# Kernel tuning notes

Measured on AMD Instinct MI355X. Metric: run time of the kernel, lower is better.

Reference implementation:

```python
import jax, jax.numpy as jnp
import numpy as np

B, S, D_MODEL = 2, 2048, 4096
N_HEADS, N_KV, HEAD_DIM = 32, 8, 128
N_GROUPS = N_HEADS // N_KV
QKV_DIM = (N_HEADS + 2 * N_KV) * HEAD_DIM


def _rope_tables(seq_len, head_dim, base=10000.0):
    inv_freq = 1.0 / (base ** (np.arange(0, head_dim, 2, dtype=np.float32) / head_dim))
    t = np.arange(seq_len, dtype=np.float32)
    freqs = np.outer(t, inv_freq)                      # [S, D/2]
    emb = np.concatenate([freqs, freqs], axis=-1)      # [S, D]
    return jnp.asarray(np.cos(emb)), jnp.asarray(np.sin(emb))


def setup_inputs() -> dict:
    key = jax.random.key(0)
    k1, k2, k3 = jax.random.split(key, 3)
    cos, sin = _rope_tables(S, HEAD_DIM)
    return {
        "hidden_states": jax.random.normal(k1, (B, S, D_MODEL), dtype=jnp.float32),
        "cos": cos,
        "sin": sin,
        "W_qkv": jax.random.normal(k2, (D_MODEL, QKV_DIM), dtype=jnp.float32) * (D_MODEL ** -0.5),
        "W_out": jax.random.normal(k3, (D_MODEL, D_MODEL), dtype=jnp.float32) * (D_MODEL ** -0.5),
    }


def _rotate_half(x):
    x1, x2 = jnp.split(x, 2, axis=-1)
    return jnp.concatenate([-x2, x1], axis=-1)


def _apply_rope(x, cos, sin):
    # x: [b, h, s, d]; cos/sin: [s, d]
    c = cos[None, None, :, :]
    s = sin[None, None, :, :]
    return x * c + _rotate_half(x) * s


def reference(hidden_states, cos, sin, W_qkv, W_out):
    b, s, _ = hidden_states.shape
    qkv = jnp.einsum("bsm,mq->bsq", hidden_states, W_qkv)
    q_end = N_HEADS * HEAD_DIM
    kv_sz = N_KV * HEAD_DIM
    q = qkv[..., :q_end].reshape(b, s, N_HEADS, HEAD_DIM).transpose(0, 2, 1, 3)
    k = qkv[..., q_end:q_end + kv_sz].reshape(b, s, N_KV, HEAD_DIM).transpose(0, 2, 1, 3)
    v = qkv[..., q_end + kv_sz:].reshape(b, s, N_KV, HEAD_DIM).transpose(0, 2, 1, 3)

    q = _apply_rope(q, cos, sin)          # [b, H, s, d]
    k = _apply_rope(k, cos, sin)          # [b, KV, s, d] (equiv. to repeat->rope->stride slice)

    # GQA without materializing repeated KV: group query heads per KV head.
    qg = q.reshape(b, N_KV, N_GROUPS, s, HEAD_DIM)
    scale = HEAD_DIM ** -0.5
    scores = jnp.einsum("bkgqd,bkpd->bkgqp", qg, k) * scale  # [b, KV, G, s, s]
    causal = jnp.tril(jnp.ones((s, s), dtype=bool))
    scores = jnp.where(causal, scores, jnp.finfo(scores.dtype).min)
    probs = jax.nn.softmax(scores, axis=-1)
    out = jnp.einsum("bkgqp,bkpd->bkgqd", probs, v)           # [b, KV, G, s, d]
    out = out.reshape(b, N_HEADS, s, HEAD_DIM).transpose(0, 2, 1, 3).reshape(b, s, D_MODEL)
    return jnp.einsum("bsm,mn->bsn", out, W_out)
```

## Files before the change

kernel.cpp:

```cpp
#include <hip/hip_runtime.h>


typedef __bf16 bf16;
typedef bf16 bf16x8 __attribute__((ext_vector_type(8)));
typedef bf16 bf16x4 __attribute__((ext_vector_type(4)));
typedef float f32x4 __attribute__((ext_vector_type(4)));
typedef unsigned int u32;
typedef u32 u32x4 __attribute__((ext_vector_type(4)));

#define B_ 2
#define S_ 2048
#define DM 4096
#define NH 32
#define NKV 8
#define HD 128
#define QKV_DIM 6144

typedef __attribute__((address_space(3))) void lds_void;
typedef const __attribute__((address_space(1))) void glb_void;

__device__ __forceinline__ void gld_lds16(const bf16* g, bf16* l) {
  __builtin_amdgcn_global_load_lds((glb_void*)g, (lds_void*)l, 16, 0, 0);
}

__device__ __forceinline__ u32 bf16bits(float x) {
  union { bf16 h; unsigned short s; } u;
  u.h = (bf16)x;
  return (u32)u.s;
}

#define BAR() __builtin_amdgcn_s_barrier()
#define VM4() asm volatile("s_waitcnt vmcnt(4)" ::: "memory")
#define VM0() asm volatile("s_waitcnt vmcnt(0)" ::: "memory")
#define PRIO1() __builtin_amdgcn_s_setprio(1)
#define PRIO0() __builtin_amdgcn_s_setprio(0)

__global__ __launch_bounds__(256) void cast_f32_bf16(const float* __restrict__ src,
                                                     bf16* __restrict__ dst, int n) {
  int i = (blockIdx.x * 256 + threadIdx.x) * 4;
  float4 v = *(const float4*)(src + i);
  bf16x4 o;
  o[0] = (bf16)v.x; o[1] = (bf16)v.y; o[2] = (bf16)v.z; o[3] = (bf16)v.w;
  *(bf16x4*)(dst + i) = o;
}

__global__ __launch_bounds__(256) void transpose_cast_w(const float* __restrict__ W,
                                                        bf16* __restrict__ Wt,
                                                        int K, int N) {
  __shared__ float tile[64][65];
  const int n0 = blockIdx.x * 64, k0 = blockIdx.y * 64;
  const int t = threadIdx.x, j = t & 63, i0 = t >> 6;
  for (int p = 0; p < 16; ++p) {
    int i = i0 + p * 4;
    tile[i][j] = W[(size_t)(k0 + i) * N + n0 + j];
  }
  __syncthreads();
  for (int p = 0; p < 16; ++p) {
    int n = i0 + p * 4;
    Wt[(size_t)(n0 + n) * K + k0 + j] = (bf16)tile[j][n];
  }
}

__global__ __launch_bounds__(256) void transpose_v(const bf16* __restrict__ qkv,
                                                   bf16* __restrict__ v_t) {
  __shared__ bf16 tile[64][65];
  const int s0 = blockIdx.x * 64;
  const int d0 = blockIdx.y * 64;
  const int bk = blockIdx.z;
  const int b = bk >> 3, kv = bk & 7;
  const int t = threadIdx.x, j = t & 63, i0 = t >> 6;
  const bf16* src = qkv + (size_t)b * S_ * QKV_DIM + 5120 + kv * HD;
  for (int p = 0; p < 16; ++p) {
    int i = i0 + p * 4;
    tile[i][j] = src[(size_t)(s0 + i) * QKV_DIM + d0 + j];
  }
  __syncthreads();
  bf16* dst = v_t + ((size_t)bk * HD + d0) * S_ + s0;
  for (int p = 0; p < 16; ++p) {
    int dd = i0 + p * 4;
    dst[(size_t)dd * S_ + j] = tile[j][dd];
  }
}

__global__ __launch_bounds__(320) void rope_kernel(const bf16* __restrict__ qkv,
                                                   const float* __restrict__ cosT,
                                                   const float* __restrict__ sinT,
                                                   bf16* __restrict__ q_r,
                                                   bf16* __restrict__ k_r) {
  const int bs = blockIdx.x;
  const int b = bs >> 11, s = bs & 2047;
  const int t = threadIdx.x;
  const int hh = t >> 3;
  const int g = (t & 7) * 8;
  const bool isQ = hh < NH;
  const bf16* row = qkv + (size_t)bs * QKV_DIM + (isQ ? hh * HD : DM + (hh - NH) * HD);
  bf16x8 xl8 = *(const bf16x8*)(row + g);
  bf16x8 xh8 = *(const bf16x8*)(row + g + 64);
  const float* cbase = cosT + (size_t)s * HD;
  const float* sbase = sinT + (size_t)s * HD;
  float cl[8], sl[8], ch[8], sh[8];
  *(float4*)(cl) = *(const float4*)(cbase + g);
  *(float4*)(cl + 4) = *(const float4*)(cbase + g + 4);
  *(float4*)(ch) = *(const float4*)(cbase + g + 64);
  *(float4*)(ch + 4) = *(const float4*)(cbase + g + 68);
  *(float4*)(sl) = *(const float4*)(sbase + g);
  *(float4*)(sl + 4) = *(const float4*)(sbase + g + 4);
  *(float4*)(sh) = *(const float4*)(sbase + g + 64);
  *(float4*)(sh + 4) = *(const float4*)(sbase + g + 68);
  const float scale = isQ ? 0.08838834764831845f : 1.0f;
  bf16x8 ol8, oh8;
#pragma unroll
  for (int j = 0; j < 8; ++j) {
    const float xl = (float)xl8[j], xh = (float)xh8[j];
    ol8[j] = (bf16)((xl * cl[j] - xh * sl[j]) * scale);
    oh8[j] = (bf16)((xh * ch[j] + xl * sh[j]) * scale);
  }
  bf16* dst = isQ ? (q_r + (((size_t)(b * NH + hh)) * S_ + s) * HD)
                  : (k_r + (((size_t)(b * NKV + (hh - NH))) * S_ + s) * HD);
  *(bf16x8*)(dst + g) = ol8;
  *(bf16x8*)(dst + g + 64) = oh8;
}

template <bool OUT_BF16, int BM, int BN>
__global__ __launch_bounds__(512, 2) void gemm_bt(const bf16* __restrict__ A,
                                                  const bf16* __restrict__ Bt,
                                                  void* __restrict__ Cout,
                                                  int M, int N, int K) {
  constexpr int MF = BM / 32;
  constexpr int NF = BN / 64;
  constexpr int NCA = BM / 128;
  constexpr int NCB = BN / 128;
  constexpr int AKH = BM * 64;
  constexpr int BKH = BN * 64;
  constexpr int BUF = 2 * (AKH + BKH);
  extern __shared__ char lds[];
  const int NT = K >> 6;

  const int nwg = gridDim.x;
  const int cpx = nwg >> 3;
  const int wg = (blockIdx.x & 7) * cpx + (blockIdx.x >> 3);
  const int nbx = N / BN;
  const int bx = wg % nbx, by = wg / nbx;
  const int m0 = by * BM, n0 = bx * BN;

  const int t = threadIdx.x;
  const int w = t >> 6, lane = t & 63;
  const int wr = w >> 2, wc = w & 3;
  const int quad = lane >> 4, c = lane & 15;

  const int aOff = (((wr * (BM / 2) + c) * 64 + quad * 16) ^ ((c & 8) << 2));
  const int bOff = 2 * AKH + ((((wc * (BN / 4) + c) * 64 + quad * 16) ^ ((c & 8) << 2)));

  const int scol = (((lane & 3) ^ ((lane >> 4) & 2)) << 3);
  const bf16* gA[NCA];
  const bf16* gB[NCB];
#pragma unroll
  for (int cc = 0; cc < NCA; ++cc)
    gA[cc] = A + (size_t)(m0 + w * (BM / 8) + cc * 16 + (lane >> 2)) * K + scol;
#pragma unroll
  for (int cc = 0; cc < NCB; ++cc)
    gB[cc] = Bt + (size_t)(n0 + w * (BN / 8) + cc * 16 + (lane >> 2)) * K + scol;

  auto stageKh = [&](int P, int kh, int ke) {
    char* ab = lds + P * BUF + kh * AKH + w * (BM * 8);
#pragma unroll
    for (int cc = 0; cc < NCA; ++cc) gld_lds16(gA[cc] + ke, (bf16*)(ab + cc * 1024));
    char* bb = lds + P * BUF + 2 * AKH + kh * BKH + w * (BN * 8);
#pragma unroll
    for (int cc = 0; cc < NCB; ++cc) gld_lds16(gB[cc] + ke, (bf16*)(bb + cc * 1024));
  };

  bf16x8 a0[MF], b0v[NF], a1[MF], b1v[NF];
  auto ldFr = [&](int P, int kh, bf16x8* av, bf16x8* bv) {
    const char* ab = lds + P * BUF + kh * AKH + aOff;
#pragma unroll
    for (int i = 0; i < MF; ++i) av[i] = *(const bf16x8*)(ab + i * 1024);
    const char* bb = lds + P * BUF + kh * BKH + bOff;
#pragma unroll
    for (int j = 0; j < NF; ++j) bv[j] = *(const bf16x8*)(bb + j * 1024);
  };

  f32x4 acc[MF][NF];
#pragma unroll
  for (int i = 0; i < MF; ++i)
#pragma unroll
    for (int j = 0; j < NF; ++j) acc[i][j] = (f32x4){0.f, 0.f, 0.f, 0.f};

  auto mfmac = [&](bf16x8* av, bf16x8* bv) {
    PRIO1();
#pragma unroll
    for (int i = 0; i < MF; ++i)
#pragma unroll
      for (int j = 0; j < NF; ++j)
        acc[i][j] = __builtin_amdgcn_mfma_f32_16x16x32_bf16(av[i], bv[j], acc[i][j], 0, 0, 0);
    PRIO0();
  };

  auto gtile = [&](int P, bool S0, bool S1) {
    BAR();
    ldFr(P, 0, a0, b0v);
    if (S0) stageKh(P ^ 1, 1, 96);
    mfmac(a0, b0v);
    ldFr(P, 1, a1, b1v);
    BAR();
    if (S1) stageKh(P, 0, 128);
    mfmac(a1, b1v);
  };

  auto adv = [&]() {
#pragma unroll
    for (int cc = 0; cc < NCA; ++cc) gA[cc] += 64;
#pragma unroll
    for (int cc = 0; cc < NCB; ++cc) gB[cc] += 64;
  };

  stageKh(0, 0, 0); stageKh(0, 1, 32); stageKh(1, 0, 64);
  VM4();

  for (int tt = 0; tt < NT - 2; tt += 2) {
    gtile(0, true, true); VM4(); adv();
    gtile(1, true, true); VM4(); adv();
  }
  gtile(0, true, false); VM0();
  gtile(1, false, false);

  const int crow = m0 + wr * (BM / 2) + quad * 4;
  const int ccol = n0 + wc * (BN / 4) + c;
#pragma unroll
  for (int mf = 0; mf < MF; ++mf)
#pragma unroll
    for (int nn = 0; nn < NF; ++nn) {
      const int row = crow + mf * 16;
      const int col = ccol + nn * 16;
      if constexpr (OUT_BF16) {
        bf16* Cp = (bf16*)Cout;
#pragma unroll
        for (int r = 0; r < 4; ++r) Cp[(size_t)(row + r) * N + col] = (bf16)acc[mf][nn][r];
      } else {
        float* Cp = (float*)Cout;
#pragma unroll
        for (int r = 0; r < 4; ++r) Cp[(size_t)(row + r) * N + col] = acc[mf][nn][r];
      }
    }
}

#define QBLK 128
#define KVB 64
#define SKS 136
#define SVS 72
__global__ __launch_bounds__(512, 4) void attn_kernel(const bf16* __restrict__ q_r,
                                                      const bf16* __restrict__ k_r,
                                                      const bf16* __restrict__ v_t,
                                                      bf16* __restrict__ attn_out) {
  __shared__ bf16 Ks[KVB * SKS];
  __shared__ bf16 Vs[128 * SVS];

  const int qb = blockIdx.x, bh = blockIdx.y;
  const int b = bh >> 5, h = bh & 31;
  const int kv = h >> 2;
  const int q0 = qb * QBLK;
  const int t = threadIdx.x, w = t >> 6, lane = t & 63;
  const int quad = lane >> 4, c = lane & 15;
  const int myq = q0 + w * 16 + c;

  const bf16* qrow = q_r + ((size_t)(b * NH + h) * S_ + myq) * HD;
  bf16x8 qf[4];
#pragma unroll
  for (int kk = 0; kk < 4; ++kk) qf[kk] = *(const bf16x8*)(qrow + quad * 8 + kk * 32);

  float m_i = -1e30f, l_i = 0.f;
  f32x4 o_acc[8];
#pragma unroll
  for (int n = 0; n < 8; ++n) o_acc[n] = (f32x4){0.f, 0.f, 0.f, 0.f};

  const bf16* kb_ptr = k_r + (size_t)(b * NKV + kv) * S_ * HD;
  const bf16* vb_ptr = v_t + (size_t)(b * NKV + kv) * HD * S_;

  const int nch = 2 * qb + 2;

  const int kkey = t >> 3, kg = (t & 7) * 8;
  const int vd = t >> 2, vk = (t & 3) * 16;
  const bf16* kp = kb_ptr + (size_t)kkey * HD + kg;
  const bf16* vp = vb_ptr + (size_t)vd * S_ + vk;

  const int src0 = c + 32 * (quad & 1);
  const int src1 = src0 + 16;
  const bool hiTile = (quad & 2) != 0;

  auto packP = [&](const float* ea, const float* eb) -> bf16x8 {
    u32 pk[4];
#pragma unroll
    for (int r = 0; r < 4; ++r) pk[r] = bf16bits(ea[r]) | (bf16bits(eb[r]) << 16);
    u32 a0[4], a1[4];
#pragma unroll
    for (int r = 0; r < 4; ++r) {
      a0[r] = (u32)__shfl((int)pk[r], src0, 64);
      a1[r] = (u32)__shfl((int)pk[r], src1, 64);
    }
    u32 w0, w1, w2, w3;
    if (hiTile) {
      w0 = (a0[0] >> 16) | (a0[1] & 0xffff0000u);
      w1 = (a0[2] >> 16) | (a0[3] & 0xffff0000u);
      w2 = (a1[0] >> 16) | (a1[1] & 0xffff0000u);
      w3 = (a1[2] >> 16) | (a1[3] & 0xffff0000u);
    } else {
      w0 = (a0[0] & 0xffffu) | (a0[1] << 16);
      w1 = (a0[2] & 0xffffu) | (a0[3] << 16);
      w2 = (a1[0] & 0xffffu) | (a1[1] << 16);
      w3 = (a1[2] & 0xffffu) | (a1[3] << 16);
    }
    return __builtin_bit_cast(bf16x8, (u32x4){w0, w1, w2, w3});
  };

  bf16x8 krg0 = *(const bf16x8*)(kp);
  bf16x8 krg1 = *(const bf16x8*)(kp + 64);
  bf16x8 vrg0 = *(const bf16x8*)(vp);
  bf16x8 vrg1 = *(const bf16x8*)(vp + 8);

  for (int ch = 0; ch < nch; ++ch) {
    const int kb = ch * KVB;
    __syncthreads();
    *(bf16x8*)(Ks + kkey * SKS + kg) = krg0;
    *(bf16x8*)(Ks + kkey * SKS + kg + 64) = krg1;
    *(bf16x8*)(Vs + vd * SVS + vk) = vrg0;
    *(bf16x8*)(Vs + vd * SVS + vk + 8) = vrg1;
    if (ch + 1 < nch) {
      kp += (size_t)KVB * HD;
      vp += KVB;
      krg0 = *(const bf16x8*)(kp);
      krg1 = *(const bf16x8*)(kp + 64);
      vrg0 = *(const bf16x8*)(vp);
      vrg1 = *(const bf16x8*)(vp + 8);
    }
    __syncthreads();

    const int wmax = q0 + w * 16 + 15;
    if (kb <= wmax) {
      const bool hi = (kb + 32 <= wmax);
      f32x4 st0 = (f32x4){0.f, 0.f, 0.f, 0.f};
      f32x4 st1 = (f32x4){0.f, 0.f, 0.f, 0.f};
      f32x4 st2 = (f32x4){0.f, 0.f, 0.f, 0.f};
      f32x4 st3 = (f32x4){0.f, 0.f, 0.f, 0.f};
#pragma unroll
      for (int kk = 0; kk < 4; ++kk) {
        bf16x8 kf0 = *(const bf16x8*)(Ks + (c) * SKS + quad * 8 + kk * 32);
        bf16x8 kf1 = *(const bf16x8*)(Ks + (16 + c) * SKS + quad * 8 + kk * 32);
        st0 = __builtin_amdgcn_mfma_f32_16x16x32_bf16(kf0, qf[kk], st0, 0, 0, 0);
        st1 = __builtin_amdgcn_mfma_f32_16x16x32_bf16(kf1, qf[kk], st1, 0, 0, 0);
      }
      if (hi) {
#pragma unroll
        for (int kk = 0; kk < 4; ++kk) {
          bf16x8 kf2 = *(const bf16x8*)(Ks + (32 + c) * SKS + quad * 8 + kk * 32);
          bf16x8 kf3 = *(const bf16x8*)(Ks + (48 + c) * SKS + quad * 8 + kk * 32);
          st2 = __builtin_amdgcn_mfma_f32_16x16x32_bf16(kf2, qf[kk], st2, 0, 0, 0);
          st3 = __builtin_amdgcn_mfma_f32_16x16x32_bf16(kf3, qf[kk], st3, 0, 0, 0);
        }
      }

      float e0[4], e1[4], e2[4], e3[4];
#pragma unroll
      for (int r = 0; r < 4; ++r) { e0[r] = st0[r]; e1[r] = st1[r]; e2[r] = st2[r]; e3[r] = st3[r]; }
      const int key0 = kb + quad * 4;
      if (kb + 31 > q0 + w * 16) {
#pragma unroll
        for (int r = 0; r < 4; ++r) {
          if (key0 + r > myq) e0[r] = -1e30f;
          if (key0 + 16 + r > myq) e1[r] = -1e30f;
        }
      }
      if (hi && kb + 63 > q0 + w * 16) {
#pragma unroll
        for (int r = 0; r < 4; ++r) {
          if (key0 + 32 + r > myq) e2[r] = -1e30f;
          if (key0 + 48 + r > myq) e3[r] = -1e30f;
        }
      }

      float mloc = fmaxf(fmaxf(fmaxf(e0[0], e0[1]), fmaxf(e0[2], e0[3])),
                         fmaxf(fmaxf(e1[0], e1[1]), fmaxf(e1[2], e1[3])));
      if (hi)
        mloc = fmaxf(mloc, fmaxf(fmaxf(fmaxf(e2[0], e2[1]), fmaxf(e2[2], e2[3])),
                                 fmaxf(fmaxf(e3[0], e3[1]), fmaxf(e3[2], e3[3]))));
      mloc = fmaxf(mloc, __shfl_xor(mloc, 16, 64));
      mloc = fmaxf(mloc, __shfl_xor(mloc, 32, 64));
      const bool defer = (__all(mloc - m_i <= 8.0f) != 0);
      const float mnew = defer ? m_i : fmaxf(m_i, mloc);
      float sum = 0.f;
#pragma unroll
      for (int r = 0; r < 4; ++r) {
        e0[r] = __expf(e0[r] - mnew); sum += e0[r];
        e1[r] = __expf(e1[r] - mnew); sum += e1[r];
      }
      if (hi) {
#pragma unroll
        for (int r = 0; r < 4; ++r) {
          e2[r] = __expf(e2[r] - mnew); sum += e2[r];
          e3[r] = __expf(e3[r] - mnew); sum += e3[r];
        }
      }
      sum += __shfl_xor(sum, 16, 64);
      sum += __shfl_xor(sum, 32, 64);
      if (!defer) {
        const float alpha = __expf(m_i - mnew);
        m_i = mnew;
        l_i = l_i * alpha + sum;
        float alpha_o[4];
#pragma unroll
        for (int r = 0; r < 4; ++r) alpha_o[r] = __shfl(alpha, quad * 4 + r, 64);
#pragma unroll
        for (int n = 0; n < 8; ++n)
#pragma unroll
          for (int r = 0; r < 4; ++r) o_acc[n][r] *= alpha_o[r];
      } else {
        l_i += sum;
      }

      bf16x8 pf0 = packP(e0, e1);
#pragma unroll
      for (int n = 0; n < 8; ++n) {
        bf16x8 vf0 = *(const bf16x8*)(Vs + (n * 16 + c) * SVS + quad * 8);
        o_acc[n] = __builtin_amdgcn_mfma_f32_16x16x32_bf16(pf0, vf0, o_acc[n], 0, 0, 0);
      }
      if (hi) {
        bf16x8 pf1 = packP(e2, e3);
#pragma unroll
        for (int n = 0; n < 8; ++n) {
          bf16x8 vf1 = *(const bf16x8*)(Vs + (n * 16 + c) * SVS + 32 + quad * 8);
          o_acc[n] = __builtin_amdgcn_mfma_f32_16x16x32_bf16(pf1, vf1, o_acc[n], 0, 0, 0);
        }
      }
    }
  }

  float l_o[4];
#pragma unroll
  for (int r = 0; r < 4; ++r) l_o[r] = __shfl(l_i, quad * 4 + r, 64);
#pragma unroll
  for (int n = 0; n < 8; ++n)
#pragma unroll
    for (int r = 0; r < 4; ++r) {
      const int row = q0 + w * 16 + quad * 4 + r;
      const float ov = o_acc[n][r] / l_o[r];
      attn_out[((size_t)b * S_ + row) * DM + h * HD + n * 16 + c] = (bf16)ov;
    }
}

extern "C" void kernel_launch(void* const* d_in, const int* in_sizes, int n_in,
                              void* d_out, int out_size, void* d_ws, size_t ws_size,
                              hipStream_t stream) {
  const float* hidden = (const float*)d_in[0];
  const float* cosT = (const float*)d_in[1];
  const float* sinT = (const float*)d_in[2];
  const float* Wqkv = (const float*)d_in[3];
  const float* Wout = (const float*)d_in[4];
  float* out = (float*)d_out;
  char* ws = (char*)d_ws;

  bf16* WqkvT = (bf16*)(ws + 0);
  bf16* q_r = (bf16*)(ws + 0);
  bf16* k_r = (bf16*)(ws + 33554432);
  bf16* WoutT = (bf16*)(ws + 50331648);
  bf16* h_bf = (bf16*)(ws + 83886080);
  bf16* attn_out = (bf16*)(ws + 83886080);
  bf16* v_t = (bf16*)(ws + 117440512);
  bf16* qkv = (bf16*)d_out;

  static bool attr_set = false;
  if (!attr_set) {
    hipFuncSetAttribute(reinterpret_cast<const void*>(&gemm_bt<true, 128, 384>),
                        hipFuncAttributeMaxDynamicSharedMemorySize, 131072);
    hipFuncSetAttribute(reinterpret_cast<const void*>(&gemm_bt<false, 256, 256>),
                        hipFuncAttributeMaxDynamicSharedMemorySize, 131072);
    attr_set = true;
  }

  cast_f32_bf16<<<dim3(16384), dim3(256), 0, stream>>>(hidden, h_bf, B_ * S_ * DM);
  transpose_cast_w<<<dim3(QKV_DIM / 64, DM / 64), dim3(256), 0, stream>>>(Wqkv, WqkvT, DM, QKV_DIM);
  transpose_cast_w<<<dim3(DM / 64, DM / 64), dim3(256), 0, stream>>>(Wout, WoutT, DM, DM);
  gemm_bt<true, 128, 384><<<dim3((QKV_DIM / 384) * ((B_ * S_) / 128)), dim3(512), 131072, stream>>>(
      h_bf, WqkvT, (void*)qkv, B_ * S_, QKV_DIM, DM);
  rope_kernel<<<dim3(B_ * S_), dim3(320), 0, stream>>>(qkv, cosT, sinT, q_r, k_r);
  transpose_v<<<dim3(S_ / 64, HD / 64, B_ * NKV), dim3(256), 0, stream>>>(qkv, v_t);
  attn_kernel<<<dim3(S_ / QBLK, B_ * NH), dim3(512), 0, stream>>>(q_r, k_r, v_t, attn_out);
  gemm_bt<false, 256, 256><<<dim3((DM / 256) * ((B_ * S_) / 256)), dim3(512), 131072, stream>>>(
      attn_out, WoutT, (void*)out, B_ * S_, DM, DM);
}
```

Baseline: 829.1 us.

## Load attention K/V tiles via direct global-to-LDS with XOR swizzle, smaller blocks

```diff
diff --git a/kernel.cpp b/kernel.cpp
--- a/kernel.cpp
+++ b/kernel.cpp
@@ -244,16 +244,14 @@
     }
 }
 
-#define QBLK 128
+#define QBLK 64
 #define KVB 64
-#define SKS 136
-#define SVS 72
-__global__ __launch_bounds__(512, 4) void attn_kernel(const bf16* __restrict__ q_r,
+__global__ __launch_bounds__(256, 2) void attn_kernel(const bf16* __restrict__ q_r,
                                                       const bf16* __restrict__ k_r,
                                                       const bf16* __restrict__ v_t,
                                                       bf16* __restrict__ attn_out) {
-  __shared__ bf16 Ks[KVB * SKS];
-  __shared__ bf16 Vs[128 * SVS];
+  __shared__ bf16 Ks[KVB * HD];
+  __shared__ bf16 Vs[HD * KVB];
 
   const int qb = blockIdx.x, bh = blockIdx.y;
   const int b = bh >> 5, h = bh & 31;
@@ -275,13 +273,14 @@
 
   const bf16* kb_ptr = k_r + (size_t)(b * NKV + kv) * S_ * HD;
   const bf16* vb_ptr = v_t + (size_t)(b * NKV + kv) * HD * S_;
-
-  const int nch = 2 * qb + 2;
-
-  const int kkey = t >> 3, kg = (t & 7) * 8;
-  const int vd = t >> 2, vk = (t & 3) * 16;
-  const bf16* kp = kb_ptr + (size_t)kkey * HD + kg;
-  const bf16* vp = vb_ptr + (size_t)vd * S_ + vk;
+  const int nch = qb + 1;
+
+  const int lr = lane >> 4, lc = lane & 15;
+  const int kcol0 = (((lc << 4) ^ (lr << 4)) >> 1);
+  const int kcol1 = (((lc << 4) ^ ((lr + 4) << 4)) >> 1);
+  const int vlr = lane >> 3, vlc = lane & 7;
+  const int vcol = (((vlc << 4) ^ (vlr << 4)) >> 1);
+  const int fxor = (c & 7) << 3;
 
   const int src0 = c + 32 * (quad & 1);
   const int src1 = src0 + 16;
@@ -312,27 +311,18 @@
     return __builtin_bit_cast(bf16x8, (u32x4){w0, w1, w2, w3});
   };
 
-  bf16x8 krg0 = *(const bf16x8*)(kp);
-  bf16x8 krg1 = *(const bf16x8*)(kp + 64);
-  bf16x8 vrg0 = *(const bf16x8*)(vp);
-  bf16x8 vrg1 = *(const bf16x8*)(vp + 8);
-
   for (int ch = 0; ch < nch; ++ch) {
     const int kb = ch * KVB;
-    __syncthreads();
-    *(bf16x8*)(Ks + kkey * SKS + kg) = krg0;
-    *(bf16x8*)(Ks + kkey * SKS + kg + 64) = krg1;
-    *(bf16x8*)(Vs + vd * SVS + vk) = vrg0;
-    *(bf16x8*)(Vs + vd * SVS + vk + 8) = vrg1;
-    if (ch + 1 < nch) {
-      kp += (size_t)KVB * HD;
-      vp += KVB;
-      krg0 = *(const bf16x8*)(kp);
-      krg1 = *(const bf16x8*)(kp + 64);
-      vrg0 = *(const bf16x8*)(vp);
-      vrg1 = *(const bf16x8*)(vp + 8);
-    }
-    __syncthreads();
+#pragma unroll
+    for (int j = 0; j < 4; ++j) {
+      const bf16* gk = kb_ptr + (size_t)(kb + w * 16 + j * 4 + lr) * HD +
+                       ((j & 1) ? kcol1 : kcol0);
+      gld_lds16(gk, Ks + (w * 16 + j * 4) * HD);
+      const bf16* gv = vb_ptr + (size_t)(w * 32 + j * 8 + vlr) * S_ + kb + vcol;
+      gld_lds16(gv, Vs + (w * 32 + j * 8) * KVB);
+    }
+    VM0();
+    BAR();
 
     const int wmax = q0 + w * 16 + 15;
     if (kb <= wmax) {
@@ -343,16 +333,18 @@
       f32x4 st3 = (f32x4){0.f, 0.f, 0.f, 0.f};
 #pragma unroll
       for (int kk = 0; kk < 4; ++kk) {
-        bf16x8 kf0 = *(const bf16x8*)(Ks + (c) * SKS + quad * 8 + kk * 32);
-        bf16x8 kf1 = *(const bf16x8*)(Ks + (16 + c) * SKS + quad * 8 + kk * 32);
+        const int kx = (quad * 8 + kk * 32) ^ fxor;
+        bf16x8 kf0 = *(const bf16x8*)(Ks + (c)*HD + kx);
+        bf16x8 kf1 = *(const bf16x8*)(Ks + (16 + c) * HD + kx);
         st0 = __builtin_amdgcn_mfma_f32_16x16x32_bf16(kf0, qf[kk], st0, 0, 0, 0);
         st1 = __builtin_amdgcn_mfma_f32_16x16x32_bf16(kf1, qf[kk], st1, 0, 0, 0);
       }
       if (hi) {
 #pragma unroll
         for (int kk = 0; kk < 4; ++kk) {
-          bf16x8 kf2 = *(const bf16x8*)(Ks + (32 + c) * SKS + quad * 8 + kk * 32);
-          bf16x8 kf3 = *(const bf16x8*)(Ks + (48 + c) * SKS + quad * 8 + kk * 32);
+          const int kx = (quad * 8 + kk * 32) ^ fxor;
+          bf16x8 kf2 = *(const bf16x8*)(Ks + (32 + c) * HD + kx);
+          bf16x8 kf3 = *(const bf16x8*)(Ks + (48 + c) * HD + kx);
           st2 = __builtin_amdgcn_mfma_f32_16x16x32_bf16(kf2, qf[kk], st2, 0, 0, 0);
           st3 = __builtin_amdgcn_mfma_f32_16x16x32_bf16(kf3, qf[kk], st3, 0, 0, 0);
         }
@@ -419,18 +411,19 @@
       bf16x8 pf0 = packP(e0, e1);
 #pragma unroll
       for (int n = 0; n < 8; ++n) {
-        bf16x8 vf0 = *(const bf16x8*)(Vs + (n * 16 + c) * SVS + quad * 8);
+        bf16x8 vf0 = *(const bf16x8*)(Vs + (n * 16 + c) * KVB + ((quad * 8) ^ fxor));
         o_acc[n] = __builtin_amdgcn_mfma_f32_16x16x32_bf16(pf0, vf0, o_acc[n], 0, 0, 0);
       }
       if (hi) {
         bf16x8 pf1 = packP(e2, e3);
 #pragma unroll
         for (int n = 0; n < 8; ++n) {
-          bf16x8 vf1 = *(const bf16x8*)(Vs + (n * 16 + c) * SVS + 32 + quad * 8);
+          bf16x8 vf1 = *(const bf16x8*)(Vs + (n * 16 + c) * KVB + ((quad * 8 + 32) ^ fxor));
           o_acc[n] = __builtin_amdgcn_mfma_f32_16x16x32_bf16(pf1, vf1, o_acc[n], 0, 0, 0);
         }
       }
     }
+    BAR();
   }
 
   float l_o[4];
@@ -482,7 +475,7 @@
       h_bf, WqkvT, (void*)qkv, B_ * S_, QKV_DIM, DM);
   rope_kernel<<<dim3(B_ * S_), dim3(320), 0, stream>>>(qkv, cosT, sinT, q_r, k_r);
   transpose_v<<<dim3(S_ / 64, HD / 64, B_ * NKV), dim3(256), 0, stream>>>(qkv, v_t);
-  attn_kernel<<<dim3(S_ / QBLK, B_ * NH), dim3(512), 0, stream>>>(q_r, k_r, v_t, attn_out);
+  attn_kernel<<<dim3(S_ / QBLK, B_ * NH), dim3(256), 0, stream>>>(q_r, k_r, v_t, attn_out);
   gemm_bt<false, 256, 256><<<dim3((DM / 256) * ((B_ * S_) / 256)), dim3(512), 131072, stream>>>(
       attn_out, WoutT, (void*)out, B_ * S_, DM, DM);
 }
```

New measurement: 819.2 us. No clear change (-1.2%).
